# Performance work log

Measured on AMD Instinct MI355X. Metric: run time of the kernel, lower is better.

Reference implementation:

```python
import jax, jax.numpy as jnp
import numpy as np

H = 16            # num_attention_heads
LN_EPS = 1e-5


def setup_inputs() -> dict:
    key = jax.random.key(0)
    ks = jax.random.split(key, 12)
    B, S, D = 2, 2048, 1024
    w_scale = 1.0 / np.sqrt(D)
    inp = {
        "hidden_states": jax.random.normal(ks[0], (B, S, D), jnp.float32),
        "attention_mask": jnp.zeros((B, 1, S, S), jnp.float32),
        "extra_attn": jax.random.normal(ks[1], (B * H, S, S), jnp.float32) * 0.02,
        "Wq": jax.random.normal(ks[2], (D, D), jnp.float32) * w_scale,
        "bq": jnp.zeros((D,), jnp.float32),
        "Wk": jax.random.normal(ks[3], (D, D), jnp.float32) * w_scale,
        "bk": jnp.zeros((D,), jnp.float32),
        "Wv": jax.random.normal(ks[4], (D, D), jnp.float32) * w_scale,
        "bv": jnp.zeros((D,), jnp.float32),
        "Wo": jax.random.normal(ks[5], (D, D), jnp.float32) * w_scale,
        "bo": jnp.zeros((D,), jnp.float32),
        "ln_gamma": jnp.ones((D,), jnp.float32),
        "ln_beta": jnp.zeros((D,), jnp.float32),
    }
    return inp


def _split_heads(x, B, S):
    # [B,S,D] -> [B,H,S,head_dim]
    D = x.shape[-1]
    return x.reshape(B, S, H, D // H).transpose(0, 2, 1, 3)


def reference(hidden_states, attention_mask, extra_attn,
              Wq, bq, Wk, bk, Wv, bv, Wo, bo, ln_gamma, ln_beta):
    B, S, D = hidden_states.shape
    head_dim = D // H
    scaling = head_dim ** -0.5

    q = (hidden_states @ Wq.T + bq) * scaling
    k = hidden_states @ Wk.T + bk
    v = hidden_states @ Wv.T + bv
    q = _split_heads(q, B, S)
    k = _split_heads(k, B, S)
    v = _split_heads(v, B, S)

    # scores: [B,H,S,S]
    scores = jnp.einsum('bhqd,bhkd->bhqk', q, k)
    scores = scores + extra_attn.reshape(B, H, S, S)
    scores = scores + attention_mask  # broadcast over heads
    probs = jax.nn.softmax(scores, axis=-1)

    attn = jnp.einsum('bhqk,bhkd->bhqd', probs, v)  # [B,H,S,hd]
    attn = attn.transpose(0, 2, 1, 3).reshape(B, S, D)
    attn_out = attn @ Wo.T + bo

    # residual + LayerNorm
    x = hidden_states + attn_out
    mu = jnp.mean(x, axis=-1, keepdims=True)
    var = jnp.mean(jnp.square(x - mu), axis=-1, keepdims=True)
    out = (x - mu) * jax.lax.rsqrt(var + LN_EPS) * ln_gamma + ln_beta
    return out
```

## Files before the change

### kernel.cpp

```cpp
#include <hip/hip_runtime.h>
#include <hip/hip_bf16.h>
#include <math.h>

typedef __bf16 bf16;
typedef __bf16 bf16x4 __attribute__((ext_vector_type(4)));
typedef __bf16 bf16x8 __attribute__((ext_vector_type(8)));
typedef float floatx4 __attribute__((ext_vector_type(4)));

#define MFMA16(a, b, c) __builtin_amdgcn_mfma_f32_16x16x32_bf16(a, b, c, 0, 0, 0)

__device__ __forceinline__ void gl_lds16(const bf16* g, bf16* l) {
  __builtin_amdgcn_global_load_lds(
      (const __attribute__((address_space(1))) void*)(g),
      (__attribute__((address_space(3))) void*)(l), 16, 0, 0);
}

__global__ __launch_bounds__(256) void k_convert(
    const float* __restrict__ hid, const float* __restrict__ wq,
    const float* __restrict__ wk, const float* __restrict__ wv,
    const float* __restrict__ wo,
    bf16* __restrict__ hidb, bf16* __restrict__ wqkvb, bf16* __restrict__ wob) {
  int g = blockIdx.x * 256 + threadIdx.x;
  int idx = g * 4;
  const float* src;
  bf16* dst;
  if (idx < 4194304) {
    src = hid + idx; dst = hidb + idx;
  } else if (idx < 7340032) {
    const float* w = (idx < 5242880) ? wq : (idx < 6291456) ? wk : wv;
    src = w + ((idx - 4194304) & 1048575);
    dst = wqkvb + (idx - 4194304);
  } else {
    src = wo + (idx - 7340032); dst = wob + (idx - 7340032);
  }
  float4 v = *(const float4*)src;
  bf16x4 o;
  o[0] = (bf16)v.x; o[1] = (bf16)v.y; o[2] = (bf16)v.z; o[3] = (bf16)v.w;
  *(bf16x4*)dst = o;
}

__global__ __launch_bounds__(256) void k_qkv_gemm(
    const bf16* __restrict__ A, const bf16* __restrict__ Bt,
    const float* __restrict__ bq, const float* __restrict__ bk,
    const float* __restrict__ bv,
    bf16* __restrict__ Qb, bf16* __restrict__ Kb, bf16* __restrict__ Vb) {
  __shared__ __align__(16) bf16 Al[128 * 64];
  __shared__ __align__(16) bf16 Bl[128 * 64];
  int tid = threadIdx.x;
  int wave = tid >> 6, L = tid & 63, quad = L >> 4, ln = L & 15;
  int m0 = blockIdx.y * 128, n0 = blockIdx.x * 128;
  int wm = (wave >> 1) * 64, wn = (wave & 1) * 64;

  floatx4 zz = {0.f, 0.f, 0.f, 0.f};
  floatx4 acc[4][4];
#pragma unroll
  for (int i = 0; i < 4; i++)
#pragma unroll
    for (int j = 0; j < 4; j++) acc[i][j] = zz;

  for (int kk = 0; kk < 1024; kk += 64) {
    __syncthreads();
#pragma unroll
    for (int u = 0; u < 4; u++) {
      int chw = u * 256 + wave * 64;
      int ch = chw + L;
      int r = ch >> 3, c8 = ch & 7;
      gl_lds16(&A[(size_t)(m0 + r) * 1024 + kk + c8 * 8], &Al[chw * 8]);
      gl_lds16(&Bt[(size_t)(n0 + r) * 1024 + kk + c8 * 8], &Bl[chw * 8]);
    }
    __syncthreads();
#pragma unroll
    for (int t = 0; t < 64; t += 32) {
      bf16x8 af[4], bfr[4];
#pragma unroll
      for (int i = 0; i < 4; i++)
        af[i] = *(const bf16x8*)&Al[(wm + i * 16 + ln) * 64 + t + quad * 8];
#pragma unroll
      for (int j = 0; j < 4; j++)
        bfr[j] = *(const bf16x8*)&Bl[(wn + j * 16 + ln) * 64 + t + quad * 8];
#pragma unroll
      for (int i = 0; i < 4; i++)
#pragma unroll
        for (int j = 0; j < 4; j++) acc[i][j] = MFMA16(af[i], bfr[j], acc[i][j]);
    }
  }
#pragma unroll
  for (int i = 0; i < 4; i++) {
    int mbase = m0 + wm + i * 16 + quad * 4;
    int b = mbase >> 11, s0 = mbase & 2047;
#pragma unroll
    for (int j = 0; j < 4; j++) {
      int n = n0 + wn + j * 16 + ln;
      int which = n >> 10, nn = n & 1023;
      float bias = (which == 0) ? bq[nn] : (which == 1) ? bk[nn] : bv[nn];
      int h = nn >> 6, d = nn & 63;
      int bh = b * 16 + h;
      if (which == 2) {
        bf16x4 v4;
#pragma unroll
        for (int r = 0; r < 4; r++) v4[r] = (bf16)(acc[i][j][r] + bias);
        *(bf16x4*)&Vb[(size_t)bh * 131072 + (size_t)d * 2048 + s0] = v4;
      } else {
#pragma unroll
        for (int r = 0; r < 4; r++) {
          float v = acc[i][j][r] + bias;
          if (which == 0)
            Qb[(size_t)bh * 131072 + (s0 + r) * 64 + d] = (bf16)(v * 0.125f);
          else
            Kb[(size_t)bh * 131072 + (s0 + r) * 64 + d] = (bf16)v;
        }
      }
    }
  }
}

__global__ __launch_bounds__(256) void k_attn(
    const bf16* __restrict__ Qb, const bf16* __restrict__ Kb,
    const bf16* __restrict__ Vb, const float* __restrict__ extra,
    const float* __restrict__ mask, bf16* __restrict__ ctx) {
  __shared__ __align__(16) bf16 Kl[2][64 * 64];
  __shared__ __align__(16) bf16 Vtl[2][64 * 64];
  __shared__ __align__(16) bf16 Pl[4][16 * 64];
  int tid = threadIdx.x;
  int wave = tid >> 6, L = tid & 63, quad = L >> 4, ln = L & 15;
  int bh = blockIdx.y, b = bh >> 4, h = bh & 15;
  int qrow = blockIdx.x * 64 + wave * 16;

  bf16x8 qf[2];
  qf[0] = *(const bf16x8*)&Qb[(size_t)bh * 131072 + (qrow + ln) * 64 + quad * 8];
  qf[1] = *(const bf16x8*)&Qb[(size_t)bh * 131072 + (qrow + ln) * 64 + 32 + quad * 8];

  float m_run[4], l_run[4];
  floatx4 zz = {0.f, 0.f, 0.f, 0.f};
  floatx4 Oacc[4];
#pragma unroll
  for (int r = 0; r < 4; r++) { m_run[r] = -INFINITY; l_run[r] = 0.f; }
#pragma unroll
  for (int dd = 0; dd < 4; dd++) Oacc[dd] = zz;

  const float* eptr[4];
  const float* mptr[4];
#pragma unroll
  for (int r = 0; r < 4; r++) {
    int q = qrow + quad * 4 + r;
    eptr[r] = extra + (size_t)bh * 4194304 + (size_t)q * 2048 + ln;
    mptr[r] = mask + (size_t)b * 4194304 + (size_t)q * 2048 + ln;
  }
  float exc[4][4];
#pragma unroll
  for (int kb = 0; kb < 4; kb++)
#pragma unroll
    for (int r = 0; r < 4; r++) exc[kb][r] = eptr[r][kb * 16];

#pragma unroll
  for (int u = 0; u < 2; u++) {
    int chw = u * 256 + wave * 64;
    int ch = chw + L;
    int row = ch >> 3, c8 = ch & 7;
    gl_lds16(&Kb[(size_t)bh * 131072 + row * 64 + c8 * 8], &Kl[0][chw * 8]);
    gl_lds16(&Vb[(size_t)bh * 131072 + (size_t)row * 2048 + c8 * 8], &Vtl[0][chw * 8]);
  }

  for (int t = 0; t < 32; t++) {
    __syncthreads();
    if (t < 31) {
      int k0n = (t + 1) * 64;
      bf16* Kn = Kl[(t + 1) & 1];
      bf16* Vn = Vtl[(t + 1) & 1];
#pragma unroll
      for (int u = 0; u < 2; u++) {
        int chw = u * 256 + wave * 64;
        int ch = chw + L;
        int row = ch >> 3, c8 = ch & 7;
        gl_lds16(&Kb[(size_t)bh * 131072 + (k0n + row) * 64 + c8 * 8], &Kn[chw * 8]);
        gl_lds16(&Vb[(size_t)bh * 131072 + (size_t)row * 2048 + k0n + c8 * 8], &Vn[chw * 8]);
      }
    }
    const bf16* Kc = Kl[t & 1];
    const bf16* Vc = Vtl[t & 1];

    floatx4 sc[4];
#pragma unroll
    for (int kb = 0; kb < 4; kb++) {
      bf16x8 kf0 = *(const bf16x8*)&Kc[(kb * 16 + ln) * 64 + quad * 8];
      bf16x8 kf1 = *(const bf16x8*)&Kc[(kb * 16 + ln) * 64 + 32 + quad * 8];
      floatx4 z = zz;
      z = MFMA16(qf[0], kf0, z);
      z = MFMA16(qf[1], kf1, z);
      sc[kb] = z;
    }
    float en[4][4];
    if (t < 31) {
#pragma unroll
      for (int kb = 0; kb < 4; kb++)
#pragma unroll
        for (int r = 0; r < 4; r++) en[kb][r] = eptr[r][64 + kb * 16];
    }
#pragma unroll
    for (int kb = 0; kb < 4; kb++)
#pragma unroll
      for (int r = 0; r < 4; r++)
        sc[kb][r] += exc[kb][r] + mptr[r][kb * 16];

#pragma unroll
    for (int r = 0; r < 4; r++) {
      float mloc = fmaxf(fmaxf(sc[0][r], sc[1][r]), fmaxf(sc[2][r], sc[3][r]));
      mloc = fmaxf(mloc, __shfl_xor(mloc, 1));
      mloc = fmaxf(mloc, __shfl_xor(mloc, 2));
      mloc = fmaxf(mloc, __shfl_xor(mloc, 4));
      mloc = fmaxf(mloc, __shfl_xor(mloc, 8));
      float m_new = fmaxf(m_run[r], mloc);
      float alpha = __expf(m_run[r] - m_new);
      m_run[r] = m_new;
      float rs = 0.f;
#pragma unroll
      for (int kb = 0; kb < 4; kb++) {
        float p = __expf(sc[kb][r] - m_new);
        sc[kb][r] = p;
        rs += p;
      }
      rs += __shfl_xor(rs, 1);
      rs += __shfl_xor(rs, 2);
      rs += __shfl_xor(rs, 4);
      rs += __shfl_xor(rs, 8);
      l_run[r] = l_run[r] * alpha + rs;
#pragma unroll
      for (int dd = 0; dd < 4; dd++) Oacc[dd][r] *= alpha;
#pragma unroll
      for (int kb = 0; kb < 4; kb++)
        Pl[wave][(quad * 4 + r) * 64 + kb * 16 + ln] = (bf16)sc[kb][r];
    }
    bf16x8 pf0 = *(const bf16x8*)&Pl[wave][ln * 64 + quad * 8];
    bf16x8 pf1 = *(const bf16x8*)&Pl[wave][ln * 64 + 32 + quad * 8];
#pragma unroll
    for (int dd = 0; dd < 4; dd++) {
      bf16x8 vf0 = *(const bf16x8*)&Vc[(dd * 16 + ln) * 64 + quad * 8];
      bf16x8 vf1 = *(const bf16x8*)&Vc[(dd * 16 + ln) * 64 + 32 + quad * 8];
      Oacc[dd] = MFMA16(pf0, vf0, Oacc[dd]);
      Oacc[dd] = MFMA16(pf1, vf1, Oacc[dd]);
    }
    if (t < 31) {
#pragma unroll
      for (int kb = 0; kb < 4; kb++)
#pragma unroll
        for (int r = 0; r < 4; r++) exc[kb][r] = en[kb][r];
#pragma unroll
      for (int r = 0; r < 4; r++) { eptr[r] += 64; mptr[r] += 64; }
    }
  }
#pragma unroll
  for (int dd = 0; dd < 4; dd++) {
#pragma unroll
    for (int r = 0; r < 4; r++) {
      int q = qrow + quad * 4 + r;
      float v = Oacc[dd][r] / l_run[r];
      ctx[((size_t)(b * 2048 + q)) * 1024 + h * 64 + dd * 16 + ln] = (bf16)v;
    }
  }
}

__global__ __launch_bounds__(256) void k_out_gemm(
    const bf16* __restrict__ A, const bf16* __restrict__ Bt,
    const float* __restrict__ bo, const float* __restrict__ hid,
    float* __restrict__ y) {
  __shared__ __align__(16) bf16 Al[64 * 64];
  __shared__ __align__(16) bf16 Bl[128 * 64];
  int tid = threadIdx.x;
  int wave = tid >> 6, L = tid & 63, quad = L >> 4, ln = L & 15;
  int m0 = blockIdx.y * 64, n0 = blockIdx.x * 128;
  int wm = (wave >> 1) * 32, wn = (wave & 1) * 64;

  floatx4 zz = {0.f, 0.f, 0.f, 0.f};
  floatx4 acc[2][4];
#pragma unroll
  for (int i = 0; i < 2; i++)
#pragma unroll
    for (int j = 0; j < 4; j++) acc[i][j] = zz;

  for (int kk = 0; kk < 1024; kk += 64) {
    __syncthreads();
#pragma unroll
    for (int u = 0; u < 2; u++) {
      int chw = u * 256 + wave * 64;
      int ch = chw + L;
      int r = ch >> 3, c8 = ch & 7;
      gl_lds16(&A[(size_t)(m0 + r) * 1024 + kk + c8 * 8], &Al[chw * 8]);
    }
#pragma unroll
    for (int u = 0; u < 4; u++) {
      int chw = u * 256 + wave * 64;
      int ch = chw + L;
      int r = ch >> 3, c8 = ch & 7;
      gl_lds16(&Bt[(size_t)(n0 + r) * 1024 + kk + c8 * 8], &Bl[chw * 8]);
    }
    __syncthreads();
#pragma unroll
    for (int t = 0; t < 64; t += 32) {
      bf16x8 af[2], bfr[4];
#pragma unroll
      for (int i = 0; i < 2; i++)
        af[i] = *(const bf16x8*)&Al[(wm + i * 16 + ln) * 64 + t + quad * 8];
#pragma unroll
      for (int j = 0; j < 4; j++)
        bfr[j] = *(const bf16x8*)&Bl[(wn + j * 16 + ln) * 64 + t + quad * 8];
#pragma unroll
      for (int i = 0; i < 2; i++)
#pragma unroll
        for (int j = 0; j < 4; j++) acc[i][j] = MFMA16(af[i], bfr[j], acc[i][j]);
    }
  }
#pragma unroll
  for (int i = 0; i < 2; i++) {
    int mbase = m0 + wm + i * 16 + quad * 4;
#pragma unroll
    for (int j = 0; j < 4; j++) {
      int n = n0 + wn + j * 16 + ln;
      float bias = bo[n];
#pragma unroll
      for (int r = 0; r < 4; r++) {
        int mm = mbase + r;
        y[(size_t)mm * 1024 + n] = acc[i][j][r] + bias + hid[(size_t)mm * 1024 + n];
      }
    }
  }
}

__global__ __launch_bounds__(256) void k_ln(float* __restrict__ y,
                                            const float* __restrict__ gamma,
                                            const float* __restrict__ beta) {
  int row = blockIdx.x, tid = threadIdx.x;
  float4 v = *(const float4*)&y[(size_t)row * 1024 + tid * 4];
  float s = v.x + v.y + v.z + v.w;
  float sq = v.x * v.x + v.y * v.y + v.z * v.z + v.w * v.w;
#pragma unroll
  for (int off = 32; off > 0; off >>= 1) {
    s += __shfl_xor(s, off);
    sq += __shfl_xor(sq, off);
  }
  __shared__ float red[8];
  int wave = tid >> 6, L = tid & 63;
  if (L == 0) { red[wave] = s; red[4 + wave] = sq; }
  __syncthreads();
  s = red[0] + red[1] + red[2] + red[3];
  sq = red[4] + red[5] + red[6] + red[7];
  float mu = s * (1.f / 1024.f);
  float var = sq * (1.f / 1024.f) - mu * mu;
  float rstd = rsqrtf(var + 1e-5f);
  float4 g = *(const float4*)&gamma[tid * 4];
  float4 be = *(const float4*)&beta[tid * 4];
  float4 o;
  o.x = (v.x - mu) * rstd * g.x + be.x;
  o.y = (v.y - mu) * rstd * g.y + be.y;
  o.z = (v.z - mu) * rstd * g.z + be.z;
  o.w = (v.w - mu) * rstd * g.w + be.w;
  *(float4*)&y[(size_t)row * 1024 + tid * 4] = o;
}

extern "C" void kernel_launch(void* const* d_in, const int* in_sizes, int n_in,
                              void* d_out, int out_size, void* d_ws,
                              size_t ws_size, hipStream_t stream) {
  const float* hid = (const float*)d_in[0];
  const float* mask = (const float*)d_in[1];
  const float* extra = (const float*)d_in[2];
  const float* Wq = (const float*)d_in[3];
  const float* bq = (const float*)d_in[4];
  const float* Wk = (const float*)d_in[5];
  const float* bk = (const float*)d_in[6];
  const float* Wv = (const float*)d_in[7];
  const float* bv = (const float*)d_in[8];
  const float* Wo = (const float*)d_in[9];
  const float* bo = (const float*)d_in[10];
  const float* gamma = (const float*)d_in[11];
  const float* beta = (const float*)d_in[12];
  float* out = (float*)d_out;

  char* ws = (char*)d_ws;
  bf16* hidb  = (bf16*)(ws);
  bf16* wqkvb = (bf16*)(ws + (8ull << 20));
  bf16* wob   = (bf16*)(ws + (14ull << 20));
  bf16* Qb    = (bf16*)(ws + (16ull << 20));
  bf16* Kb    = (bf16*)(ws + (24ull << 20));
  bf16* Vb    = (bf16*)(ws + (32ull << 20));
  bf16* ctx   = (bf16*)(ws + (40ull << 20));

  k_convert<<<8192, 256, 0, stream>>>(hid, Wq, Wk, Wv, Wo, hidb, wqkvb, wob);
  k_qkv_gemm<<<dim3(24, 32), 256, 0, stream>>>(hidb, wqkvb, bq, bk, bv, Qb, Kb, Vb);
  k_attn<<<dim3(32, 32), 256, 0, stream>>>(Qb, Kb, Vb, extra, mask, ctx);
  k_out_gemm<<<dim3(8, 64), 256, 0, stream>>>(ctx, wob, bo, hid, out);
  k_ln<<<4096, 256, 0, stream>>>(out, gamma, beta);
}
```

Measured before the change: 932.2 us.

## Stage extra_attn tiles through LDS with async global_load_lds double buffering

The attention kernel now streams the fp32 extra_attn bias tile for each 64x64 key block into a double-buffered LDS array using global_load_lds. This runs alongside the K/V prefetch, replacing per-thread strided scalar global loads held in registers. The mask keeps its register prefetch, and launch bounds now request 2 blocks per SM. LDS use grows by 32KB per block, which may limit occupancy, and adds LDS reads in exchange for coalesced 16-byte loads of the largest input stream.

```diff
diff --git a/kernel.cpp b/kernel.cpp
--- a/kernel.cpp
+++ b/kernel.cpp
@@ -9,7 +9,7 @@
 
 #define MFMA16(a, b, c) __builtin_amdgcn_mfma_f32_16x16x32_bf16(a, b, c, 0, 0, 0)
 
-__device__ __forceinline__ void gl_lds16(const bf16* g, bf16* l) {
+__device__ __forceinline__ void gl_lds16(const void* g, void* l) {
   __builtin_amdgcn_global_load_lds(
       (const __attribute__((address_space(1))) void*)(g),
       (__attribute__((address_space(3))) void*)(l), 16, 0, 0);
@@ -114,17 +114,20 @@
   }
 }
 
-__global__ __launch_bounds__(256) void k_attn(
+__global__ __launch_bounds__(256, 2) void k_attn(
     const bf16* __restrict__ Qb, const bf16* __restrict__ Kb,
     const bf16* __restrict__ Vb, const float* __restrict__ extra,
     const float* __restrict__ mask, bf16* __restrict__ ctx) {
   __shared__ __align__(16) bf16 Kl[2][64 * 64];
   __shared__ __align__(16) bf16 Vtl[2][64 * 64];
+  __shared__ __align__(16) float El[2][64 * 64];
   __shared__ __align__(16) bf16 Pl[4][16 * 64];
   int tid = threadIdx.x;
   int wave = tid >> 6, L = tid & 63, quad = L >> 4, ln = L & 15;
-  int bh = blockIdx.y, b = bh >> 4, h = bh & 15;
-  int qrow = blockIdx.x * 64 + wave * 16;
+  int bh = blockIdx.y, b = bh >> 4;
+  int q0 = blockIdx.x * 64;
+  int qrow = q0 + wave * 16;
+  int h = bh & 15;
 
   bf16x8 qf[2];
   qf[0] = *(const bf16x8*)&Qb[(size_t)bh * 131072 + (qrow + ln) * 64 + quad * 8];
@@ -138,19 +141,11 @@
 #pragma unroll
   for (int dd = 0; dd < 4; dd++) Oacc[dd] = zz;
 
-  const float* eptr[4];
+  const size_t ebase = (size_t)bh * 4194304;
   const float* mptr[4];
 #pragma unroll
-  for (int r = 0; r < 4; r++) {
-    int q = qrow + quad * 4 + r;
-    eptr[r] = extra + (size_t)bh * 4194304 + (size_t)q * 2048 + ln;
-    mptr[r] = mask + (size_t)b * 4194304 + (size_t)q * 2048 + ln;
-  }
-  float exc[4][4];
-#pragma unroll
-  for (int kb = 0; kb < 4; kb++)
-#pragma unroll
-    for (int r = 0; r < 4; r++) exc[kb][r] = eptr[r][kb * 16];
+  for (int r = 0; r < 4; r++)
+    mptr[r] = mask + (size_t)b * 4194304 + (size_t)(qrow + quad * 4 + r) * 2048 + ln;
 
 #pragma unroll
   for (int u = 0; u < 2; u++) {
@@ -160,6 +155,18 @@
     gl_lds16(&Kb[(size_t)bh * 131072 + row * 64 + c8 * 8], &Kl[0][chw * 8]);
     gl_lds16(&Vb[(size_t)bh * 131072 + (size_t)row * 2048 + c8 * 8], &Vtl[0][chw * 8]);
   }
+#pragma unroll
+  for (int u = 0; u < 4; u++) {
+    int chw = u * 256 + wave * 64;
+    int ch = chw + L;
+    int row = ch >> 4, c = ch & 15;
+    gl_lds16(&extra[ebase + (size_t)(q0 + row) * 2048 + c * 4], &El[0][chw * 4]);
+  }
+  float mcur[4][4];
+#pragma unroll
+  for (int kb = 0; kb < 4; kb++)
+#pragma unroll
+    for (int r = 0; r < 4; r++) mcur[kb][r] = mptr[r][kb * 16];
 
   for (int t = 0; t < 32; t++) {
     __syncthreads();
@@ -167,6 +174,7 @@
       int k0n = (t + 1) * 64;
       bf16* Kn = Kl[(t + 1) & 1];
       bf16* Vn = Vtl[(t + 1) & 1];
+      float* En = El[(t + 1) & 1];
 #pragma unroll
       for (int u = 0; u < 2; u++) {
         int chw = u * 256 + wave * 64;
@@ -175,9 +183,24 @@
         gl_lds16(&Kb[(size_t)bh * 131072 + (k0n + row) * 64 + c8 * 8], &Kn[chw * 8]);
         gl_lds16(&Vb[(size_t)bh * 131072 + (size_t)row * 2048 + k0n + c8 * 8], &Vn[chw * 8]);
       }
+#pragma unroll
+      for (int u = 0; u < 4; u++) {
+        int chw = u * 256 + wave * 64;
+        int ch = chw + L;
+        int row = ch >> 4, c = ch & 15;
+        gl_lds16(&extra[ebase + (size_t)(q0 + row) * 2048 + k0n + c * 4], &En[chw * 4]);
+      }
+    }
+    float mn[4][4];
+    if (t < 31) {
+#pragma unroll
+      for (int kb = 0; kb < 4; kb++)
+#pragma unroll
+        for (int r = 0; r < 4; r++) mn[kb][r] = mptr[r][64 + kb * 16];
     }
     const bf16* Kc = Kl[t & 1];
     const bf16* Vc = Vtl[t & 1];
+    const float* Ec = El[t & 1];
 
     floatx4 sc[4];
 #pragma unroll
@@ -189,18 +212,11 @@
       z = MFMA16(qf[1], kf1, z);
       sc[kb] = z;
     }
-    float en[4][4];
-    if (t < 31) {
-#pragma unroll
-      for (int kb = 0; kb < 4; kb++)
-#pragma unroll
-        for (int r = 0; r < 4; r++) en[kb][r] = eptr[r][64 + kb * 16];
-    }
 #pragma unroll
     for (int kb = 0; kb < 4; kb++)
 #pragma unroll
       for (int r = 0; r < 4; r++)
-        sc[kb][r] += exc[kb][r] + mptr[r][kb * 16];
+        sc[kb][r] += Ec[(wave * 16 + quad * 4 + r) * 64 + kb * 16 + ln] + mcur[kb][r];
 
 #pragma unroll
     for (int r = 0; r < 4; r++) {
@@ -243,9 +259,9 @@
 #pragma unroll
       for (int kb = 0; kb < 4; kb++)
 #pragma unroll
-        for (int r = 0; r < 4; r++) exc[kb][r] = en[kb][r];
-#pragma unroll
-      for (int r = 0; r < 4; r++) { eptr[r] += 64; mptr[r] += 64; }
+        for (int r = 0; r < 4; r++) mcur[kb][r] = mn[kb][r];
+#pragma unroll
+      for (int r = 0; r < 4; r++) mptr[r] += 64;
     }
   }
 #pragma unroll
```

Measured after the change: 924.3 us. No clear change (-0.8%).
